# Kernel optimization log

Hardware: AMD Instinct MI355X
Metric: run time of the kernel (lower is better)

Reference implementation:

```python
import jax, jax.numpy as jnp
import numpy as np

SHAPES = [(4, 48, 48), (2, 24, 24), (1, 12, 12), (1, 6, 6)]  # (D,H,W) per level
B, E, NH, NL, NP, DF, NLAYERS = 2, 256, 8, 4, 4, 1024, 6
HD = E // NH
LEVEL_SIZES = [d * h * w for d, h, w in SHAPES]
LEVEL_START = [0] + [int(s) for s in np.cumsum(LEVEL_SIZES)[:-1]]
S = int(sum(LEVEL_SIZES))
PARAM_KEYS = ['W_off', 'b_off', 'W_attn', 'b_attn', 'W_val', 'b_val', 'W_out', 'b_out',
              'ln1_g', 'ln1_b', 'W_ff1', 'b_ff1', 'W_ff2', 'b_ff2', 'ln2_g', 'ln2_b']


def setup_inputs() -> dict:
    key = jax.random.key(0)
    ks = jax.random.split(key, 32)
    inp = {}
    for i, (d, h, w) in enumerate(SHAPES):
        inp[f'feat{i}'] = jax.random.normal(ks[i], (B, E, d, h, w), jnp.float32)
        inp[f'pos{i}'] = jax.random.normal(ks[4 + i], (B, E, d, h, w), jnp.float32)
    inp['level_embed'] = jax.random.normal(ks[8], (NL, E), jnp.float32)
    nrm = lambda k, shape, s: jax.random.normal(k, shape, jnp.float32) * s
    inp['W_off'] = nrm(ks[9], (NLAYERS, E, NH * NL * NP * 3), 0.01)
    inp['b_off'] = nrm(ks[10], (NLAYERS, NH * NL * NP * 3), 1.0)
    inp['W_attn'] = nrm(ks[11], (NLAYERS, E, NH * NL * NP), 0.02)
    inp['b_attn'] = jnp.zeros((NLAYERS, NH * NL * NP), jnp.float32)
    inp['W_val'] = nrm(ks[12], (NLAYERS, E, E), E ** -0.5)
    inp['b_val'] = jnp.zeros((NLAYERS, E), jnp.float32)
    inp['W_out'] = nrm(ks[13], (NLAYERS, E, E), E ** -0.5)
    inp['b_out'] = jnp.zeros((NLAYERS, E), jnp.float32)
    inp['ln1_g'] = jnp.ones((NLAYERS, E), jnp.float32)
    inp['ln1_b'] = jnp.zeros((NLAYERS, E), jnp.float32)
    inp['W_ff1'] = nrm(ks[14], (NLAYERS, E, DF), E ** -0.5)
    inp['b_ff1'] = jnp.zeros((NLAYERS, DF), jnp.float32)
    inp['W_ff2'] = nrm(ks[15], (NLAYERS, DF, E), DF ** -0.5)
    inp['b_ff2'] = jnp.zeros((NLAYERS, E), jnp.float32)
    inp['ln2_g'] = jnp.ones((NLAYERS, E), jnp.float32)
    inp['ln2_b'] = jnp.zeros((NLAYERS, E), jnp.float32)
    return inp


def _layer_norm(x, g, b):
    m = jnp.mean(x, -1, keepdims=True)
    v = jnp.mean((x - m) ** 2, -1, keepdims=True)
    return (x - m) * jax.lax.rsqrt(v + 1e-5) * g + b


def _ref_points():
    # all-zero padding masks -> valid_ratios == 1, so reference points are the
    # normalized voxel centers, identical across levels. Returns (S, 3) in (x, y, z).
    refs = []
    for (D, H, W) in SHAPES:
        z = (jnp.arange(D, dtype=jnp.float32) + 0.5) / D
        y = (jnp.arange(H, dtype=jnp.float32) + 0.5) / H
        x = (jnp.arange(W, dtype=jnp.float32) + 0.5) / W
        zz, yy, xx = jnp.meshgrid(z, y, x, indexing='ij')
        refs.append(jnp.stack([xx.ravel(), yy.ravel(), zz.ravel()], -1))
    return jnp.concatenate(refs, 0)


def _sample_level(v, coords, w, D, H, W):
    # v: (B, NH, N_lvl, HD) flattened level values
    # coords: (B, NH, S, NP, 3) pixel-space coords (x, y, z), align_corners=False convention
    # w: (B, NH, S, NP) attention weights (folded into trilinear corner weights)
    cx, cy, cz = coords[..., 0], coords[..., 1], coords[..., 2]
    x0, y0, z0 = jnp.floor(cx), jnp.floor(cy), jnp.floor(cz)
    fx, fy, fz = cx - x0, cy - y0, cz - z0
    Bq, Hq, Sq, Pq = w.shape
    acc = jnp.zeros((Bq, Hq, Sq, HD), v.dtype)
    for dz in (0, 1):
        wz = fz if dz else 1.0 - fz
        iz = z0 + dz
        for dy in (0, 1):
            wy = fy if dy else 1.0 - fy
            iy = y0 + dy
            for dx in (0, 1):
                wx = fx if dx else 1.0 - fx
                ix = x0 + dx
                valid = (ix >= 0) & (ix < W) & (iy >= 0) & (iy < H) & (iz >= 0) & (iz < D)
                wgt = w * wx * wy * wz * valid  # zero-padding outside the volume
                idx = ((jnp.clip(iz, 0, D - 1) * H + jnp.clip(iy, 0, H - 1)) * W
                       + jnp.clip(ix, 0, W - 1)).astype(jnp.int32)
                g = jnp.take_along_axis(v, idx.reshape(Bq, Hq, Sq * Pq)[..., None], axis=2)
                g = g.reshape(Bq, Hq, Sq, Pq, HD)
                acc = acc + jnp.einsum('bhsp,bhspd->bhsd', wgt, g)
    return acc


def _deform_attn(x, pos, ref, normalizer, p, sample_fn):
    B_, S_, _ = x.shape
    q = x + pos
    value = (x @ p['W_val'] + p['b_val']).reshape(B_, S_, NH, HD).transpose(0, 2, 1, 3)
    off = (q @ p['W_off'] + p['b_off']).reshape(B_, S_, NH, NL, NP, 3)
    attn = jax.nn.softmax((q @ p['W_attn'] + p['b_attn']).reshape(B_, S_, NH, NL * NP), -1)
    attn = attn.reshape(B_, S_, NH, NL, NP)
    # normalized sampling locations in [0,1]^3 (x, y, z)
    loc = ref[None, :, None, None, None, :] + off / normalizer[None, None, None, :, None, :]
    out = jnp.zeros((B_, NH, S_, HD), x.dtype)
    for lvl, (D, H, W) in enumerate(SHAPES):
        s0, n = LEVEL_START[lvl], LEVEL_SIZES[lvl]
        v = value[:, :, s0:s0 + n]
        size = jnp.array([W, H, D], x.dtype)
        coords = (loc[:, :, :, lvl] * size - 0.5).transpose(0, 2, 1, 3, 4)  # (B,NH,S,NP,3)
        w = attn[:, :, :, lvl].transpose(0, 2, 1, 3)  # (B,NH,S,NP)
        out = out + sample_fn(v, coords, w, D, H, W)
    out = out.transpose(0, 2, 1, 3).reshape(B_, S_, E)
    return out @ p['W_out'] + p['b_out']


def _encoder_layer(x, pos, ref, normalizer, p, sample_fn):
    x = _layer_norm(x + _deform_attn(x, pos, ref, normalizer, p, sample_fn),
                    p['ln1_g'], p['ln1_b'])
    h = jax.nn.relu(x @ p['W_ff1'] + p['b_ff1']) @ p['W_ff2'] + p['b_ff2']
    return _layer_norm(x + h, p['ln2_g'], p['ln2_b'])


def _forward(feats, poss, level_embed, params, sample_fn):
    x = jnp.concatenate([f.reshape(f.shape[0], E, -1).transpose(0, 2, 1) for f in feats], axis=1)
    pos = jnp.concatenate(
        [poss[l].reshape(poss[l].shape[0], E, -1).transpose(0, 2, 1) + level_embed[l]
         for l in range(NL)], axis=1)
    ref = _ref_points()
    normalizer = jnp.array([[w, h, d] for d, h, w in SHAPES], jnp.float32)  # (NL,3) (x,y,z)
    for l in range(NLAYERS):
        p = {k: params[k][l] for k in PARAM_KEYS}
        x = _encoder_layer(x, pos, ref, normalizer, p, sample_fn)
    return x


def reference(feat0, feat1, feat2, feat3, pos0, pos1, pos2, pos3, level_embed,
              W_off, b_off, W_attn, b_attn, W_val, b_val, W_out, b_out,
              ln1_g, ln1_b, W_ff1, b_ff1, W_ff2, b_ff2, ln2_g, ln2_b):
    params = dict(W_off=W_off, b_off=b_off, W_attn=W_attn, b_attn=b_attn,
                  W_val=W_val, b_val=b_val, W_out=W_out, b_out=b_out,
                  ln1_g=ln1_g, ln1_b=ln1_b, W_ff1=W_ff1, b_ff1=b_ff1,
                  W_ff2=W_ff2, b_ff2=b_ff2, ln2_g=ln2_g, ln2_b=ln2_b)
    return _forward([feat0, feat1, feat2, feat3], [pos0, pos1, pos2, pos3],
                    level_embed, params, _sample_level)
```

## Files before the change

kernel.cpp:

```cpp
#include <hip/hip_runtime.h>

#define S_TOT   10548
#define M_ROWS  21096
#define M_PAD   21120
#define E_DIM   256
#define NH_DIM  8
#define HD_DIM  32
#define DF_DIM  1024
#define NLAYERS 6

typedef unsigned short ushort_t;
typedef __attribute__((ext_vector_type(8))) short bf16x8;
typedef __attribute__((ext_vector_type(4))) float f32x4;

__device__ inline ushort_t f2bf(float f) {
    unsigned u = __float_as_uint(f);
    u += 0x7FFF + ((u >> 16) & 1);
    return (ushort_t)(u >> 16);
}
__device__ inline float bf2f(ushort_t h) {
    return __uint_as_float(((unsigned)h) << 16);
}
__device__ inline f32x4 up2(unsigned a, unsigned b) {
    f32x4 v;
    v.x = __uint_as_float(a << 16);
    v.y = __uint_as_float(a & 0xffff0000u);
    v.z = __uint_as_float(b << 16);
    v.w = __uint_as_float(b & 0xffff0000u);
    return v;
}
__device__ inline void gload16(const ushort_t* g, ushort_t* l) {
    __builtin_amdgcn_global_load_lds(
        (const __attribute__((address_space(1))) void*)g,
        (__attribute__((address_space(3))) void*)l, 16, 0, 0);
}

__global__ __launch_bounds__(256)
void assemble_kernel(const float* __restrict__ f0, const float* __restrict__ p0,
                     const float* __restrict__ f1, const float* __restrict__ p1,
                     const float* __restrict__ f2, const float* __restrict__ p2,
                     const float* __restrict__ f3, const float* __restrict__ p3,
                     const float* __restrict__ lemb,
                     float* __restrict__ x, ushort_t* __restrict__ posb,
                     ushort_t* __restrict__ xb, ushort_t* __restrict__ qb)
{
    int idx = blockIdx.x * 256 + threadIdx.x;
    int e = idx & (E_DIM - 1);
    int r = idx >> 8;
    int b = (r >= S_TOT) ? 1 : 0;
    int s = r - b * S_TOT;
    const float* f; const float* p; int lvl, j, n;
    if (s < 9216)       { lvl = 0; j = s;         n = 9216; f = f0; p = p0; }
    else if (s < 10368) { lvl = 1; j = s - 9216;  n = 1152; f = f1; p = p1; }
    else if (s < 10512) { lvl = 2; j = s - 10368; n = 144;  f = f2; p = p2; }
    else                { lvl = 3; j = s - 10512; n = 36;   f = f3; p = p3; }
    size_t o = (size_t)(b * E_DIM + e) * n + j;
    float xv = f[o];
    float pv = p[o] + lemb[lvl * E_DIM + e];
    x[idx]    = xv;
    posb[idx] = f2bf(pv);
    xb[idx]   = f2bf(xv);
    qb[idx]   = f2bf(xv + pv);
}

__global__ __launch_bounds__(256)
void transpose_cvt_kernel(const float* __restrict__ src, ushort_t* __restrict__ dst,
                          int K, int N, int dstLayerStride, int dstRowOff)
{
    __shared__ float tile[32][33];
    int l  = blockIdx.z;
    int n0 = blockIdx.x * 32, k0 = blockIdx.y * 32;
    int tx = threadIdx.x & 31, ty = threadIdx.x >> 5;
    const float* s = src + (size_t)l * K * N;
    ushort_t* d    = dst + (size_t)l * dstLayerStride + (size_t)dstRowOff * K;
    #pragma unroll
    for (int i = 0; i < 32; i += 8)
        tile[ty + i][tx] = s[(size_t)(k0 + ty + i) * N + n0 + tx];
    __syncthreads();
    #pragma unroll
    for (int i = 0; i < 32; i += 8)
        d[(size_t)(n0 + ty + i) * K + k0 + tx] = f2bf(tile[tx][ty + i]);
}

__global__ __launch_bounds__(256, 2)
void gemm_part1(const ushort_t* __restrict__ A0, const ushort_t* __restrict__ A1,
                const ushort_t* __restrict__ BtBase,
                const float* __restrict__ b1, const float* __restrict__ b2,
                const float* __restrict__ b3,
                ushort_t* __restrict__ O1, ushort_t* __restrict__ O2,
                ushort_t* __restrict__ O3, int M)
{
    __shared__ short As[2][64 * 32];
    __shared__ short Bs[2][256 * 32];
    const int K = 256;
    int t    = threadIdx.x;
    int sup  = blockIdx.x;
    int row0 = blockIdx.y * 64;
    int lane = t & 63;
    int w    = t >> 6;
    int wn   = w * 64;
    const int quad = lane >> 4, lrow = lane & 15;

    const ushort_t* A  = (sup != 0) ? A1 : A0;
    const ushort_t* Bt = BtBase + (size_t)sup * 256 * K;

    f32x4 acc[4][4];
    #pragma unroll
    for (int i = 0; i < 4; ++i)
        #pragma unroll
        for (int j = 0; j < 4; ++j)
            acc[i][j] = (f32x4){0.f, 0.f, 0.f, 0.f};

    int srow = lane >> 2;
    const int sw = (((lane & 3) ^ ((lane >> 3) & 3)) * 8);
    const int rs = ((quad ^ ((lrow >> 1) & 3)) * 8);
    const ushort_t* Ag = A + (size_t)(row0 + w * 16 + srow) * K + sw;
    const ushort_t* Bg = Bt + (size_t)(w * 64 + srow) * K + sw;

    gload16(Ag, (ushort_t*)&As[0][(w * 16) * 32]);
    #pragma unroll
    for (int q = 0; q < 4; ++q)
        gload16(Bg + (size_t)(q * 16) * K,
                (ushort_t*)&Bs[0][(w * 64 + q * 16) * 32]);

    #pragma unroll
    for (int k0 = 0; k0 < K; k0 += 32) {
        const int cur = (k0 >> 5) & 1;
        __syncthreads();
        if (k0 + 32 < K) {
            const int nxt = cur ^ 1;
            gload16(Ag + k0 + 32, (ushort_t*)&As[nxt][(w * 16) * 32]);
            #pragma unroll
            for (int q = 0; q < 4; ++q)
                gload16(Bg + (size_t)(q * 16) * K + k0 + 32,
                        (ushort_t*)&Bs[nxt][(w * 64 + q * 16) * 32]);
        }
        bf16x8 af[4], bfr[4];
        #pragma unroll
        for (int i = 0; i < 4; ++i)
            af[i] = *(const bf16x8*)&As[cur][(i * 16 + lrow) * 32 + rs];
        #pragma unroll
        for (int j = 0; j < 4; ++j)
            bfr[j] = *(const bf16x8*)&Bs[cur][(wn + j * 16 + lrow) * 32 + rs];
        #pragma unroll
        for (int i = 0; i < 4; ++i)
            #pragma unroll
            for (int j = 0; j < 4; ++j)
                acc[i][j] = __builtin_amdgcn_mfma_f32_16x16x32_bf16(af[i], bfr[j], acc[i][j], 0, 0, 0);
    }

    #pragma unroll
    for (int j = 0; j < 4; ++j) {
        int col = wn + j * 16 + lrow;
        float bia = (sup == 0) ? b1[col]
                  : (sup == 1) ? b2[col]
                  : (col < 128) ? b2[256 + col] : b3[col - 128];
        #pragma unroll
        for (int i = 0; i < 4; ++i)
            #pragma unroll
            for (int rg = 0; rg < 4; ++rg) {
                int row = row0 + i * 16 + quad * 4 + rg;
                if (row < M) {
                    float v = acc[i][j][rg] + bia;
                    if (sup == 0) {
                        int b = (row >= S_TOT) ? 1 : 0;
                        int s = row - b * S_TOT;
                        O1[(((size_t)(b * NH_DIM + (col >> 5))) * S_TOT + s) * HD_DIM + (col & 31)] = f2bf(v);
                    } else if (sup == 2 && col >= 128) {
                        int acol = col - 128;
                        O3[((size_t)(acol >> 4) * M_ROWS + row) * 16 + (acol & 15)] = f2bf(v);
                    } else {
                        int ocol = (sup == 1) ? col : 256 + col;
                        int hh = (ocol * 1366) >> 16;
                        O2[((size_t)hh * M_ROWS + row) * 48 + (ocol - hh * 48)] = f2bf(v);
                    }
                }
            }
    }
}

__global__ __launch_bounds__(256, 2)
void gemm_ln(const ushort_t* __restrict__ A, const ushort_t* __restrict__ Bt,
             const float* __restrict__ bias,
             float* __restrict__ x, ushort_t* __restrict__ xb,
             const float* __restrict__ lng, const float* __restrict__ lnb,
             int M)
{
    __shared__ short As[2][64 * 32];
    __shared__ short Bs[2][256 * 32];
    __shared__ float red1[64 * 5];
    __shared__ float red2[64 * 5];
    const int K = 256;
    int t    = threadIdx.x;
    int row0 = blockIdx.x * 64;
    int lane = t & 63;
    int w    = t >> 6;
    int wn   = w * 64;
    const int quad = lane >> 4, lrow = lane & 15;

    f32x4 acc[4][4];
    #pragma unroll
    for (int i = 0; i < 4; ++i)
        #pragma unroll
        for (int j = 0; j < 4; ++j)
            acc[i][j] = (f32x4){0.f, 0.f, 0.f, 0.f};

    int srow = lane >> 2;
    const int sw = (((lane & 3) ^ ((lane >> 3) & 3)) * 8);
    const int rs = ((quad ^ ((lrow >> 1) & 3)) * 8);
    const ushort_t* Ag = A + (size_t)(row0 + w * 16 + srow) * K + sw;
    const ushort_t* Bg = Bt + (size_t)(w * 64 + srow) * K + sw;

    gload16(Ag, (ushort_t*)&As[0][(w * 16) * 32]);
    #pragma unroll
    for (int q = 0; q < 4; ++q)
        gload16(Bg + (size_t)(q * 16) * K,
                (ushort_t*)&Bs[0][(w * 64 + q * 16) * 32]);

    #pragma unroll
    for (int k0 = 0; k0 < K; k0 += 32) {
        const int cur = (k0 >> 5) & 1;
        __syncthreads();
        if (k0 + 32 < K) {
            const int nxt = cur ^ 1;
            gload16(Ag + k0 + 32, (ushort_t*)&As[nxt][(w * 16) * 32]);
            #pragma unroll
            for (int q = 0; q < 4; ++q)
                gload16(Bg + (size_t)(q * 16) * K + k0 + 32,
                        (ushort_t*)&Bs[nxt][(w * 64 + q * 16) * 32]);
        }
        bf16x8 af[4], bfr[4];
        #pragma unroll
        for (int i = 0; i < 4; ++i)
            af[i] = *(const bf16x8*)&As[cur][(i * 16 + lrow) * 32 + rs];
        #pragma unroll
        for (int j = 0; j < 4; ++j)
            bfr[j] = *(const bf16x8*)&Bs[cur][(wn + j * 16 + lrow) * 32 + rs];
        #pragma unroll
        for (int i = 0; i < 4; ++i)
            #pragma unroll
            for (int j = 0; j < 4; ++j)
                acc[i][j] = __builtin_amdgcn_mfma_f32_16x16x32_bf16(af[i], bfr[j], acc[i][j], 0, 0, 0);
    }

    float gj[4], bj[4], bi[4];
    #pragma unroll
    for (int j = 0; j < 4; ++j) {
        int col = wn + j * 16 + lrow;
        gj[j] = lng[col];
        bj[j] = lnb[col];
        bi[j] = bias[col];
    }

    #pragma unroll
    for (int i = 0; i < 4; ++i)
        #pragma unroll
        for (int rg = 0; rg < 4; ++rg) {
            int row = row0 + i * 16 + quad * 4 + rg;
            #pragma unroll
            for (int j = 0; j < 4; ++j) {
                int col = wn + j * 16 + lrow;
                float xres = (row < M) ? x[(size_t)row * 256 + col] : 0.f;
                acc[i][j][rg] += bi[j] + xres;
            }
            float p1 = acc[i][0][rg] + acc[i][1][rg] + acc[i][2][rg] + acc[i][3][rg];
            float p2 = acc[i][0][rg] * acc[i][0][rg] + acc[i][1][rg] * acc[i][1][rg]
                     + acc[i][2][rg] * acc[i][2][rg] + acc[i][3][rg] * acc[i][3][rg];
            p1 += __shfl_xor(p1, 1); p2 += __shfl_xor(p2, 1);
            p1 += __shfl_xor(p1, 2); p2 += __shfl_xor(p2, 2);
            p1 += __shfl_xor(p1, 4); p2 += __shfl_xor(p2, 4);
            p1 += __shfl_xor(p1, 8); p2 += __shfl_xor(p2, 8);
            if (lrow == 0) {
                int rl = i * 16 + quad * 4 + rg;
                red1[rl * 5 + w] = p1;
                red2[rl * 5 + w] = p2;
            }
        }
    __syncthreads();

    #pragma unroll
    for (int i = 0; i < 4; ++i)
        #pragma unroll
        for (int rg = 0; rg < 4; ++rg) {
            int rl = i * 16 + quad * 4 + rg;
            float S1 = red1[rl * 5 + 0] + red1[rl * 5 + 1] + red1[rl * 5 + 2] + red1[rl * 5 + 3];
            float S2 = red2[rl * 5 + 0] + red2[rl * 5 + 1] + red2[rl * 5 + 2] + red2[rl * 5 + 3];
            float mean = S1 * (1.f / 256);
            float rstd = rsqrtf(S2 * (1.f / 256) - mean * mean + 1e-5f);
            int row = row0 + rl;
            if (row < M) {
                #pragma unroll
                for (int j = 0; j < 4; ++j) {
                    int col = wn + j * 16 + lrow;
                    float out = (acc[i][j][rg] - mean) * rstd * gj[j] + bj[j];
                    size_t o = (size_t)row * 256 + col;
                    x[o]  = out;
                    xb[o] = f2bf(out);
                }
            }
        }
}

__global__ __launch_bounds__(256, 2)
void ffn_kernel(const ushort_t* __restrict__ Axb, const ushort_t* __restrict__ W1t,
                const ushort_t* __restrict__ W2t,
                const float* __restrict__ bias1, const float* __restrict__ bias2,
                float* __restrict__ x, ushort_t* __restrict__ xb,
                ushort_t* __restrict__ qb, const ushort_t* __restrict__ posb,
                const float* __restrict__ lng, const float* __restrict__ lnb,
                int M)
{
    __shared__ short As[2][64 * 32];
    __shared__ short Bs[2][256 * 32];
    __shared__ short Hs[64 * 264];
    __shared__ float red1[64 * 5];
    __shared__ float red2[64 * 5];
    const int K = 256;
    int t    = threadIdx.x;
    int row0 = blockIdx.x * 64;
    int lane = t & 63;
    int w    = t >> 6;
    int wn   = w * 64;
    const int quad = lane >> 4, lrow = lane & 15;
    int srow = lane >> 2;
    const int sw = (((lane & 3) ^ ((lane >> 3) & 3)) * 8);
    const int rs = ((quad ^ ((lrow >> 1) & 3)) * 8);

    f32x4 acc[4][4];
    #pragma unroll
    for (int i = 0; i < 4; ++i)
        #pragma unroll
        for (int j = 0; j < 4; ++j)
            acc[i][j] = (f32x4){0.f, 0.f, 0.f, 0.f};

    const ushort_t* Ag = Axb + (size_t)(row0 + w * 16 + srow) * K + sw;

    for (int c = 0; c < 4; ++c) {
        f32x4 hh[4][4];
        #pragma unroll
        for (int i = 0; i < 4; ++i)
            #pragma unroll
            for (int j = 0; j < 4; ++j)
                hh[i][j] = (f32x4){0.f, 0.f, 0.f, 0.f};

        const ushort_t* B1g = W1t + (size_t)(c * 256 + w * 64 + srow) * K + sw;

        __syncthreads();
        gload16(Ag, (ushort_t*)&As[0][(w * 16) * 32]);
        #pragma unroll
        for (int q = 0; q < 4; ++q)
            gload16(B1g + (size_t)(q * 16) * K,
                    (ushort_t*)&Bs[0][(w * 64 + q * 16) * 32]);

        #pragma unroll
        for (int k0 = 0; k0 < K; k0 += 32) {
            const int cur = (k0 >> 5) & 1;
            __syncthreads();
            if (k0 + 32 < K) {
                const int nxt = cur ^ 1;
                gload16(Ag + k0 + 32, (ushort_t*)&As[nxt][(w * 16) * 32]);
                #pragma unroll
                for (int q = 0; q < 4; ++q)
                    gload16(B1g + (size_t)(q * 16) * K + k0 + 32,
                            (ushort_t*)&Bs[nxt][(w * 64 + q * 16) * 32]);
            }
            bf16x8 af[4], bfr[4];
            #pragma unroll
            for (int i = 0; i < 4; ++i)
                af[i] = *(const bf16x8*)&As[cur][(i * 16 + lrow) * 32 + rs];
            #pragma unroll
            for (int j = 0; j < 4; ++j)
                bfr[j] = *(const bf16x8*)&Bs[cur][(wn + j * 16 + lrow) * 32 + rs];
            #pragma unroll
            for (int i = 0; i < 4; ++i)
                #pragma unroll
                for (int j = 0; j < 4; ++j)
                    hh[i][j] = __builtin_amdgcn_mfma_f32_16x16x32_bf16(af[i], bfr[j], hh[i][j], 0, 0, 0);
        }

        #pragma unroll
        for (int j = 0; j < 4; ++j) {
            int col = wn + j * 16 + lrow;
            float b1v = bias1[c * 256 + col];
            #pragma unroll
            for (int i = 0; i < 4; ++i)
                #pragma unroll
                for (int rg = 0; rg < 4; ++rg) {
                    int rl = i * 16 + quad * 4 + rg;
                    Hs[rl * 264 + col] = f2bf(fmaxf(hh[i][j][rg] + b1v, 0.f));
                }
        }
        __syncthreads();

        const ushort_t* B2g = W2t + (size_t)(w * 64 + srow) * 1024 + c * 256 + sw;
        #pragma unroll
        for (int q = 0; q < 4; ++q)
            gload16(B2g + (size_t)(q * 16) * 1024,
                    (ushort_t*)&Bs[0][(w * 64 + q * 16) * 32]);

        #pragma unroll
        for (int k0 = 0; k0 < 256; k0 += 32) {
            const int cur = (k0 >> 5) & 1;
            __syncthreads();
            if (k0 + 32 < 256) {
                const int nxt = cur ^ 1;
                #pragma unroll
                for (int q = 0; q < 4; ++q)
                    gload16(B2g + (size_t)(q * 16) * 1024 + k0 + 32,
                            (ushort_t*)&Bs[nxt][(w * 64 + q * 16) * 32]);
            }
            bf16x8 af[4], bfr[4];
            #pragma unroll
            for (int i = 0; i < 4; ++i)
                af[i] = *(const bf16x8*)&Hs[(i * 16 + lrow) * 264 + k0 + quad * 8];
            #pragma unroll
            for (int j = 0; j < 4; ++j)
                bfr[j] = *(const bf16x8*)&Bs[cur][(wn + j * 16 + lrow) * 32 + rs];
            #pragma unroll
            for (int i = 0; i < 4; ++i)
                #pragma unroll
                for (int j = 0; j < 4; ++j)
                    acc[i][j] = __builtin_amdgcn_mfma_f32_16x16x32_bf16(af[i], bfr[j], acc[i][j], 0, 0, 0);
        }
    }

    float gj[4], bj[4], bi[4];
    #pragma unroll
    for (int j = 0; j < 4; ++j) {
        int col = wn + j * 16 + lrow;
        gj[j] = lng[col];
        bj[j] = lnb[col];
        bi[j] = bias2[col];
    }

    #pragma unroll
    for (int i = 0; i < 4; ++i)
        #pragma unroll
        for (int rg = 0; rg < 4; ++rg) {
            int row = row0 + i * 16 + quad * 4 + rg;
            #pragma unroll
            for (int j = 0; j < 4; ++j) {
                int col = wn + j * 16 + lrow;
                float xres = (row < M) ? x[(size_t)row * 256 + col] : 0.f;
                acc[i][j][rg] += bi[j] + xres;
            }
            float p1 = acc[i][0][rg] + acc[i][1][rg] + acc[i][2][rg] + acc[i][3][rg];
            float p2 = acc[i][0][rg] * acc[i][0][rg] + acc[i][1][rg] * acc[i][1][rg]
                     + acc[i][2][rg] * acc[i][2][rg] + acc[i][3][rg] * acc[i][3][rg];
            p1 += __shfl_xor(p1, 1); p2 += __shfl_xor(p2, 1);
            p1 += __shfl_xor(p1, 2); p2 += __shfl_xor(p2, 2);
            p1 += __shfl_xor(p1, 4); p2 += __shfl_xor(p2, 4);
            p1 += __shfl_xor(p1, 8); p2 += __shfl_xor(p2, 8);
            if (lrow == 0) {
                int rl = i * 16 + quad * 4 + rg;
                red1[rl * 5 + w] = p1;
                red2[rl * 5 + w] = p2;
            }
        }
    __syncthreads();

    #pragma unroll
    for (int i = 0; i < 4; ++i)
        #pragma unroll
        for (int rg = 0; rg < 4; ++rg) {
            int rl = i * 16 + quad * 4 + rg;
            float S1 = red1[rl * 5 + 0] + red1[rl * 5 + 1] + red1[rl * 5 + 2] + red1[rl * 5 + 3];
            float S2 = red2[rl * 5 + 0] + red2[rl * 5 + 1] + red2[rl * 5 + 2] + red2[rl * 5 + 3];
            float mean = S1 * (1.f / 256);
            float rstd = rsqrtf(S2 * (1.f / 256) - mean * mean + 1e-5f);
            int row = row0 + rl;
            if (row < M) {
                #pragma unroll
                for (int j = 0; j < 4; ++j) {
                    int col = wn + j * 16 + lrow;
                    float out = (acc[i][j][rg] - mean) * rstd * gj[j] + bj[j];
                    size_t o = (size_t)row * 256 + col;
                    x[o]  = out;
                    xb[o] = f2bf(out);
                    qb[o] = f2bf(out + bf2f(posb[o]));
                }
            }
        }
}

__global__ __launch_bounds__(256, 4)
void sample_kernel(const ushort_t* __restrict__ valueb,
                   const ushort_t* __restrict__ offh,
                   const ushort_t* __restrict__ attnh,
                   ushort_t* __restrict__ sampb)
{
    __shared__ float wrec[16 * 168];
    __shared__ int   idxA[16 * 40];

    const int LD_[4]  = {4, 2, 1, 1};
    const int LH_[4]  = {48, 24, 12, 6};
    const int LW_[4]  = {48, 24, 12, 6};
    const int LS0_[4] = {0, 9216, 10368, 10512};

    int t   = threadIdx.x;
    int gl  = t >> 4;
    int sub = t & 15;
    int h   = blockIdx.x;
    int r   = blockIdx.y * 16 + gl;
    bool valid = (r < M_ROWS);
    if (!valid) r = M_ROWS - 1;
    int b   = (r >= S_TOT) ? 1 : 0;
    int s   = r - b * S_TOT;

    float rx, ry, rz;
    {
        int j;
        if (s < 9216)       { j = s;         int qx = j % 48; int q2 = j / 48; int qy = q2 % 48; int qz = q2 / 48;
                              rx = (qx + 0.5f) * (1.f/48); ry = (qy + 0.5f) * (1.f/48); rz = (qz + 0.5f) * (1.f/4); }
        else if (s < 10368) { j = s - 9216;  int qx = j % 24; int q2 = j / 24; int qy = q2 % 24; int qz = q2 / 24;
                              rx = (qx + 0.5f) * (1.f/24); ry = (qy + 0.5f) * (1.f/24); rz = (qz + 0.5f) * (1.f/2); }
        else if (s < 10512) { j = s - 10368; int qx = j % 12; int qy = j / 12;
                              rx = (qx + 0.5f) * (1.f/12); ry = (qy + 0.5f) * (1.f/12); rz = 0.5f; }
        else                { j = s - 10512; int qx = j % 6;  int qy = j / 6;
                              rx = (qx + 0.5f) * (1.f/6);  ry = (qy + 0.5f) * (1.f/6);  rz = 0.5f; }
    }

    {
        int p = sub;
        float lg = bf2f(attnh[((size_t)h * M_ROWS + r) * 16 + p]);
        float mx = lg;
        mx = fmaxf(mx, __shfl_xor(mx, 1));
        mx = fmaxf(mx, __shfl_xor(mx, 2));
        mx = fmaxf(mx, __shfl_xor(mx, 4));
        mx = fmaxf(mx, __shfl_xor(mx, 8));
        float e = __expf(lg - mx);
        float sm = e;
        sm += __shfl_xor(sm, 1);
        sm += __shfl_xor(sm, 2);
        sm += __shfl_xor(sm, 4);
        sm += __shfl_xor(sm, 8);
        float aw = e / sm;

        int lvl = p >> 2;
        const int Dl = LD_[lvl], Hl = LH_[lvl], Wl = LW_[lvl];
        size_t base3 = ((size_t)h * M_ROWS + r) * 48 + p * 3;
        float cx = rx * Wl + bf2f(offh[base3 + 0]) - 0.5f;
        float cy = ry * Hl + bf2f(offh[base3 + 1]) - 0.5f;
        float cz = rz * Dl + bf2f(offh[base3 + 2]) - 0.5f;
        float xf = floorf(cx), yf = floorf(cy), zf = floorf(cz);
        float fx = cx - xf, fy = cy - yf, fz = cz - zf;
        int x0 = (int)xf, y0 = (int)yf, z0 = (int)zf;
        float wx0 = ((unsigned)x0       < (unsigned)Wl) ? 1.f - fx : 0.f;
        float wx1 = ((unsigned)(x0 + 1) < (unsigned)Wl) ? fx       : 0.f;
        float wy0 = ((unsigned)y0       < (unsigned)Hl) ? 1.f - fy : 0.f;
        float wy1 = ((unsigned)(y0 + 1) < (unsigned)Hl) ? fy       : 0.f;
        float wz0 = ((unsigned)z0       < (unsigned)Dl) ? (1.f - fz) * aw : 0.f;
        float wz1 = ((unsigned)(z0 + 1) < (unsigned)Dl) ? fz * aw       : 0.f;
        int xc = min(max(x0, -1), Wl - 1);
        int yc = min(max(y0, -1), Hl - 1);
        int zc = min(max(z0, -1), Dl - 1);
        int idx = LS0_[lvl] + (zc * Hl + yc) * Wl + xc;

        float* wp = &wrec[gl * 168 + p * 8];
        *(f32x4*)wp       = (f32x4){wz0 * wy0 * wx0, wz0 * wy0 * wx1,
                                    wz0 * wy1 * wx0, wz0 * wy1 * wx1};
        *(f32x4*)(wp + 4) = (f32x4){wz1 * wy0 * wx0, wz1 * wy0 * wx1,
                                    wz1 * wy1 * wx0, wz1 * wy1 * wx1};
        idxA[gl * 40 + p] = idx;
    }
    __syncthreads();

    int q  = sub & 3;
    int cr = sub >> 2;
    int dy = cr >> 1, dx = cr & 1;
    const ushort_t* vb = valueb + ((size_t)(b * NH_DIM + h) * S_TOT) * HD_DIM + q * 8;
    f32x4 accA = (f32x4){0.f, 0.f, 0.f, 0.f};
    f32x4 accB = (f32x4){0.f, 0.f, 0.f, 0.f};

    #pragma unroll
    for (int p = 0; p < 16; ++p) {
        const int lvl = p >> 2;
        const int Wl = LW_[lvl];
        const int HW = LH_[lvl] * LW_[lvl];
        float w0 = wrec[gl * 168 + p * 8 + cr];
        float w1 = wrec[gl * 168 + p * 8 + 4 + cr];
        int idx = idxA[gl * 40 + p] + dy * Wl + dx;
        const ushort_t* cb = vb + (long long)idx * HD_DIM;
        uint4 u0 = *(const uint4*)cb;
        uint4 u1 = *(const uint4*)(cb + HW * HD_DIM);
        accA += w0 * up2(u0.x, u0.y);
        accB += w0 * up2(u0.z, u0.w);
        accA += w1 * up2(u1.x, u1.y);
        accB += w1 * up2(u1.z, u1.w);
    }

    accA.x += __shfl_xor(accA.x, 4); accA.y += __shfl_xor(accA.y, 4);
    accA.z += __shfl_xor(accA.z, 4); accA.w += __shfl_xor(accA.w, 4);
    accB.x += __shfl_xor(accB.x, 4); accB.y += __shfl_xor(accB.y, 4);
    accB.z += __shfl_xor(accB.z, 4); accB.w += __shfl_xor(accB.w, 4);
    accA.x += __shfl_xor(accA.x, 8); accA.y += __shfl_xor(accA.y, 8);
    accA.z += __shfl_xor(accA.z, 8); accA.w += __shfl_xor(accA.w, 8);
    accB.x += __shfl_xor(accB.x, 8); accB.y += __shfl_xor(accB.y, 8);
    accB.z += __shfl_xor(accB.z, 8); accB.w += __shfl_xor(accB.w, 8);

    if (cr == 0 && valid) {
        ushort4 o1, o2;
        o1.x = f2bf(accA.x); o1.y = f2bf(accA.y); o1.z = f2bf(accA.z); o1.w = f2bf(accA.w);
        o2.x = f2bf(accB.x); o2.y = f2bf(accB.y); o2.z = f2bf(accB.z); o2.w = f2bf(accB.w);
        ushort_t* op = sampb + (size_t)r * E_DIM + h * HD_DIM + q * 8;
        *(ushort4*)op       = o1;
        *(ushort4*)(op + 4) = o2;
    }
}

extern "C" void kernel_launch(void* const* d_in, const int* in_sizes, int n_in,
                              void* d_out, int out_size, void* d_ws, size_t ws_size,
                              hipStream_t stream)
{
    const float* f0     = (const float*)d_in[0];
    const float* p0     = (const float*)d_in[1];
    const float* f1     = (const float*)d_in[2];
    const float* p1     = (const float*)d_in[3];
    const float* f2     = (const float*)d_in[4];
    const float* p2     = (const float*)d_in[5];
    const float* f3     = (const float*)d_in[6];
    const float* p3     = (const float*)d_in[7];
    const float* lemb   = (const float*)d_in[8];
    const float* W_off  = (const float*)d_in[9];
    const float* b_off  = (const float*)d_in[10];
    const float* W_attn = (const float*)d_in[11];
    const float* b_attn = (const float*)d_in[12];
    const float* W_val  = (const float*)d_in[13];
    const float* b_val  = (const float*)d_in[14];
    const float* W_out  = (const float*)d_in[15];
    const float* b_out  = (const float*)d_in[16];
    const float* ln1_g  = (const float*)d_in[17];
    const float* ln1_b  = (const float*)d_in[18];
    const float* W_ff1  = (const float*)d_in[19];
    const float* b_ff1  = (const float*)d_in[20];
    const float* W_ff2  = (const float*)d_in[21];
    const float* b_ff2  = (const float*)d_in[22];
    const float* ln2_g  = (const float*)d_in[23];
    const float* ln2_b  = (const float*)d_in[24];

    float* x = (float*)d_out;
    char*  w = (char*)d_ws;

    ushort_t* posb   = (ushort_t*)(w + 0);
    ushort_t* valueb = (ushort_t*)(w + 21626880 + 262144);
    char*     region =            (w + 34525184);
    ushort_t* offh   = (ushort_t*)(region);
    ushort_t* attnh  = (ushort_t*)(region + 16220160);
    ushort_t* sampb  = (ushort_t*)(region + 21626880);
    ushort_t* xb     = (ushort_t*)(w + 77778944);
    ushort_t* qb     = (ushort_t*)(w + 88592384);
    ushort_t* wb     = (ushort_t*)(w + 99405824);

    ushort_t* Wc_t = wb;
    ushort_t* Wp_t = wb + 1179648;
    ushort_t* W1_t = wb + 1572864;
    ushort_t* W2_t = wb + 3145728;

    dim3 blk(256);

    transpose_cvt_kernel<<<dim3(8, 8, 6),  blk, 0, stream>>>(W_val,  Wc_t, 256, 256,  196608, 0);
    transpose_cvt_kernel<<<dim3(12, 8, 6), blk, 0, stream>>>(W_off,  Wc_t, 256, 384,  196608, 256);
    transpose_cvt_kernel<<<dim3(4, 8, 6),  blk, 0, stream>>>(W_attn, Wc_t, 256, 128,  196608, 640);
    transpose_cvt_kernel<<<dim3(8, 8, 6),  blk, 0, stream>>>(W_out,  Wp_t, 256, 256,   65536, 0);
    transpose_cvt_kernel<<<dim3(32, 8, 6), blk, 0, stream>>>(W_ff1,  W1_t, 256, 1024, 262144, 0);
    transpose_cvt_kernel<<<dim3(8, 32, 6), blk, 0, stream>>>(W_ff2,  W2_t, 1024, 256, 262144, 0);

    assemble_kernel<<<(M_ROWS * E_DIM) / 256, blk, 0, stream>>>(
        f0, p0, f1, p1, f2, p2, f3, p3, lemb, x, posb, xb, qb);

    const int MT = M_PAD / 64;
    const int SB = (M_ROWS + 15) / 16;
    for (int l = 0; l < NLAYERS; ++l) {
        gemm_part1<<<dim3(3, MT), blk, 0, stream>>>(
            xb, qb, Wc_t + l * 196608,
            b_val + l * 256, b_off + l * 384, b_attn + l * 128,
            valueb, offh, attnh, M_ROWS);
        sample_kernel<<<dim3(NH_DIM, SB), blk, 0, stream>>>(valueb, offh, attnh, sampb);
        gemm_ln<<<MT, blk, 0, stream>>>(
            sampb, Wp_t + l * 65536, b_out + l * 256,
            x, xb, ln1_g + l * 256, ln1_b + l * 256, M_ROWS);
        ffn_kernel<<<MT, blk, 0, stream>>>(
            xb, W1_t + l * 262144, W2_t + l * 262144,
            b_ff1 + l * 1024, b_ff2 + l * 256,
            x, xb, qb, posb,
            ln2_g + l * 256, ln2_b + l * 256, M_ROWS);
    }
}
```

Measured before the change: 1.168 ms.

## Halve row tile in LN GEMM and FFN kernels, tile-transpose input assembly

The row tile of gemm_ln and ffn_kernel drops from 64 to 32 rows. This halves accumulators and LDS use, reuses the A buffer for the reduction scratch, raises the occupancy hint to 4 blocks, and doubles the grid so more blocks cover the CUs. The assemble kernel now does an LDS-tiled transpose, so reads from the channel-major feature and pos tensors are coalesced. The price is that each weight tile is reused across fewer rows, so weight traffic from L2 grows.

```diff
diff --git a/kernel.cpp b/kernel.cpp
--- a/kernel.cpp
+++ b/kernel.cpp
@@ -44,23 +44,49 @@
                      float* __restrict__ x, ushort_t* __restrict__ posb,
                      ushort_t* __restrict__ xb, ushort_t* __restrict__ qb)
 {
-    int idx = blockIdx.x * 256 + threadIdx.x;
-    int e = idx & (E_DIM - 1);
-    int r = idx >> 8;
-    int b = (r >= S_TOT) ? 1 : 0;
-    int s = r - b * S_TOT;
-    const float* f; const float* p; int lvl, j, n;
-    if (s < 9216)       { lvl = 0; j = s;         n = 9216; f = f0; p = p0; }
-    else if (s < 10368) { lvl = 1; j = s - 9216;  n = 1152; f = f1; p = p1; }
-    else if (s < 10512) { lvl = 2; j = s - 10368; n = 144;  f = f2; p = p2; }
-    else                { lvl = 3; j = s - 10512; n = 36;   f = f3; p = p3; }
-    size_t o = (size_t)(b * E_DIM + e) * n + j;
-    float xv = f[o];
-    float pv = p[o] + lemb[lvl * E_DIM + e];
-    x[idx]    = xv;
-    posb[idx] = f2bf(pv);
-    xb[idx]   = f2bf(xv);
-    qb[idx]   = f2bf(xv + pv);
+    __shared__ float tf[32][33];
+    __shared__ float tp[32][33];
+
+    int tb = blockIdx.x;
+    int e0 = blockIdx.y * 32;
+    int b  = blockIdx.z;
+    int lvl, j0, n, s0; const float* f; const float* p;
+    if (tb < 288)      { lvl = 0; j0 = tb * 32;         n = 9216; s0 = 0;     f = f0; p = p0; }
+    else if (tb < 324) { lvl = 1; j0 = (tb - 288) * 32; n = 1152; s0 = 9216;  f = f1; p = p1; }
+    else if (tb < 329) { lvl = 2; j0 = (tb - 324) * 32; n = 144;  s0 = 10368; f = f2; p = p2; }
+    else               { lvl = 3; j0 = (tb - 329) * 32; n = 36;   s0 = 10512; f = f3; p = p3; }
+
+    int tx = threadIdx.x & 31, ty = threadIdx.x >> 5;
+    bool jv = (j0 + tx) < n;
+    size_t base = (size_t)(b * E_DIM + e0) * n + j0 + tx;
+    #pragma unroll
+    for (int i = 0; i < 4; ++i) {
+        int e = ty + i * 8;
+        float fv = 0.f, pv = 0.f;
+        if (jv) {
+            fv = f[base + (size_t)e * n];
+            pv = p[base + (size_t)e * n];
+        }
+        tf[e][tx] = fv;
+        tp[e][tx] = pv;
+    }
+    __syncthreads();
+
+    float lv = lemb[lvl * E_DIM + e0 + tx];
+    #pragma unroll
+    for (int i = 0; i < 4; ++i) {
+        int jl = ty + i * 8;
+        if (j0 + jl < n) {
+            int r = b * S_TOT + s0 + j0 + jl;
+            float xv = tf[tx][jl];
+            float pv = tp[tx][jl] + lv;
+            size_t o = (size_t)r * E_DIM + e0 + tx;
+            x[o]    = xv;
+            posb[o] = f2bf(pv);
+            xb[o]   = f2bf(xv);
+            qb[o]   = f2bf(xv + pv);
+        }
+    }
 }
 
 __global__ __launch_bounds__(256)
@@ -179,28 +205,28 @@
     }
 }
 
-__global__ __launch_bounds__(256, 2)
+__global__ __launch_bounds__(256, 4)
 void gemm_ln(const ushort_t* __restrict__ A, const ushort_t* __restrict__ Bt,
              const float* __restrict__ bias,
              float* __restrict__ x, ushort_t* __restrict__ xb,
              const float* __restrict__ lng, const float* __restrict__ lnb,
              int M)
 {
-    __shared__ short As[2][64 * 32];
+    __shared__ short As[2][32 * 32];
     __shared__ short Bs[2][256 * 32];
-    __shared__ float red1[64 * 5];
-    __shared__ float red2[64 * 5];
+    float* red1 = (float*)&As[0][0];
+    float* red2 = red1 + 32 * 5;
     const int K = 256;
     int t    = threadIdx.x;
-    int row0 = blockIdx.x * 64;
+    int row0 = blockIdx.x * 32;
     int lane = t & 63;
     int w    = t >> 6;
     int wn   = w * 64;
     const int quad = lane >> 4, lrow = lane & 15;
 
-    f32x4 acc[4][4];
-    #pragma unroll
-    for (int i = 0; i < 4; ++i)
+    f32x4 acc[2][4];
+    #pragma unroll
+    for (int i = 0; i < 2; ++i)
         #pragma unroll
         for (int j = 0; j < 4; ++j)
             acc[i][j] = (f32x4){0.f, 0.f, 0.f, 0.f};
@@ -211,7 +237,7 @@
     const ushort_t* Ag = A + (size_t)(row0 + w * 16 + srow) * K + sw;
     const ushort_t* Bg = Bt + (size_t)(w * 64 + srow) * K + sw;
 
-    gload16(Ag, (ushort_t*)&As[0][(w * 16) * 32]);
+    if (w < 2) gload16(Ag, (ushort_t*)&As[0][(w * 16) * 32]);
     #pragma unroll
     for (int q = 0; q < 4; ++q)
         gload16(Bg + (size_t)(q * 16) * K,
@@ -223,21 +249,21 @@
         __syncthreads();
         if (k0 + 32 < K) {
             const int nxt = cur ^ 1;
-            gload16(Ag + k0 + 32, (ushort_t*)&As[nxt][(w * 16) * 32]);
+            if (w < 2) gload16(Ag + k0 + 32, (ushort_t*)&As[nxt][(w * 16) * 32]);
             #pragma unroll
             for (int q = 0; q < 4; ++q)
                 gload16(Bg + (size_t)(q * 16) * K + k0 + 32,
                         (ushort_t*)&Bs[nxt][(w * 64 + q * 16) * 32]);
         }
-        bf16x8 af[4], bfr[4];
-        #pragma unroll
-        for (int i = 0; i < 4; ++i)
+        bf16x8 af[2], bfr[4];
+        #pragma unroll
+        for (int i = 0; i < 2; ++i)
             af[i] = *(const bf16x8*)&As[cur][(i * 16 + lrow) * 32 + rs];
         #pragma unroll
         for (int j = 0; j < 4; ++j)
             bfr[j] = *(const bf16x8*)&Bs[cur][(wn + j * 16 + lrow) * 32 + rs];
         #pragma unroll
-        for (int i = 0; i < 4; ++i)
+        for (int i = 0; i < 2; ++i)
             #pragma unroll
             for (int j = 0; j < 4; ++j)
                 acc[i][j] = __builtin_amdgcn_mfma_f32_16x16x32_bf16(af[i], bfr[j], acc[i][j], 0, 0, 0);
@@ -253,7 +279,7 @@
     }
 
     #pragma unroll
-    for (int i = 0; i < 4; ++i)
+    for (int i = 0; i < 2; ++i)
         #pragma unroll
         for (int rg = 0; rg < 4; ++rg) {
             int row = row0 + i * 16 + quad * 4 + rg;
@@ -279,7 +305,7 @@
     __syncthreads();
 
     #pragma unroll
-    for (int i = 0; i < 4; ++i)
+    for (int i = 0; i < 2; ++i)
         #pragma unroll
         for (int rg = 0; rg < 4; ++rg) {
             int rl = i * 16 + quad * 4 + rg;
@@ -310,14 +336,14 @@
                 const float* __restrict__ lng, const float* __restrict__ lnb,
                 int M)
 {
-    __shared__ short As[2][64 * 32];
+    __shared__ short As[2][32 * 32];
     __shared__ short Bs[2][256 * 32];
-    __shared__ short Hs[64 * 264];
-    __shared__ float red1[64 * 5];
-    __shared__ float red2[64 * 5];
+    __shared__ short Hs[32 * 264];
+    float* red1 = (float*)&As[0][0];
+    float* red2 = red1 + 32 * 5;
     const int K = 256;
     int t    = threadIdx.x;
-    int row0 = blockIdx.x * 64;
+    int row0 = blockIdx.x * 32;
     int lane = t & 63;
     int w    = t >> 6;
     int wn   = w * 64;
@@ -326,9 +352,9 @@
     const int sw = (((lane & 3) ^ ((lane >> 3) & 3)) * 8);
     const int rs = ((quad ^ ((lrow >> 1) & 3)) * 8);
 
-    f32x4 acc[4][4];
-    #pragma unroll
-    for (int i = 0; i < 4; ++i)
+    f32x4 acc[2][4];
+    #pragma unroll
+    for (int i = 0; i < 2; ++i)
         #pragma unroll
         for (int j = 0; j < 4; ++j)
             acc[i][j] = (f32x4){0.f, 0.f, 0.f, 0.f};
@@ -336,9 +362,9 @@
     const ushort_t* Ag = Axb + (size_t)(row0 + w * 16 + srow) * K + sw;
 
     for (int c = 0; c < 4; ++c) {
-        f32x4 hh[4][4];
-        #pragma unroll
-        for (int i = 0; i < 4; ++i)
+        f32x4 hh[2][4];
+        #pragma unroll
+        for (int i = 0; i < 2; ++i)
             #pragma unroll
             for (int j = 0; j < 4; ++j)
                 hh[i][j] = (f32x4){0.f, 0.f, 0.f, 0.f};
@@ -346,7 +372,7 @@
         const ushort_t* B1g = W1t + (size_t)(c * 256 + w * 64 + srow) * K + sw;
 
         __syncthreads();
-        gload16(Ag, (ushort_t*)&As[0][(w * 16) * 32]);
+        if (w < 2) gload16(Ag, (ushort_t*)&As[0][(w * 16) * 32]);
         #pragma unroll
         for (int q = 0; q < 4; ++q)
             gload16(B1g + (size_t)(q * 16) * K,
@@ -358,21 +384,21 @@
             __syncthreads();
             if (k0 + 32 < K) {
                 const int nxt = cur ^ 1;
-                gload16(Ag + k0 + 32, (ushort_t*)&As[nxt][(w * 16) * 32]);
+                if (w < 2) gload16(Ag + k0 + 32, (ushort_t*)&As[nxt][(w * 16) * 32]);
                 #pragma unroll
                 for (int q = 0; q < 4; ++q)
                     gload16(B1g + (size_t)(q * 16) * K + k0 + 32,
                             (ushort_t*)&Bs[nxt][(w * 64 + q * 16) * 32]);
             }
-            bf16x8 af[4], bfr[4];
-            #pragma unroll
-            for (int i = 0; i < 4; ++i)
+            bf16x8 af[2], bfr[4];
+            #pragma unroll
+            for (int i = 0; i < 2; ++i)
                 af[i] = *(const bf16x8*)&As[cur][(i * 16 + lrow) * 32 + rs];
             #pragma unroll
             for (int j = 0; j < 4; ++j)
                 bfr[j] = *(const bf16x8*)&Bs[cur][(wn + j * 16 + lrow) * 32 + rs];
             #pragma unroll
-            for (int i = 0; i < 4; ++i)
+            for (int i = 0; i < 2; ++i)
                 #pragma unroll
                 for (int j = 0; j < 4; ++j)
                     hh[i][j] = __builtin_amdgcn_mfma_f32_16x16x32_bf16(af[i], bfr[j], hh[i][j], 0, 0, 0);
@@ -383,7 +409,7 @@
             int col = wn + j * 16 + lrow;
             float b1v = bias1[c * 256 + col];
             #pragma unroll
-            for (int i = 0; i < 4; ++i)
+            for (int i = 0; i < 2; ++i)
                 #pragma unroll
                 for (int rg = 0; rg < 4; ++rg) {
                     int rl = i * 16 + quad * 4 + rg;
@@ -409,15 +435,15 @@
                     gload16(B2g + (size_t)(q * 16) * 1024 + k0 + 32,
                             (ushort_t*)&Bs[nxt][(w * 64 + q * 16) * 32]);
             }
-            bf16x8 af[4], bfr[4];
-            #pragma unroll
-            for (int i = 0; i < 4; ++i)
+            bf16x8 af[2], bfr[4];
+            #pragma unroll
+            for (int i = 0; i < 2; ++i)
                 af[i] = *(const bf16x8*)&Hs[(i * 16 + lrow) * 264 + k0 + quad * 8];
             #pragma unroll
             for (int j = 0; j < 4; ++j)
                 bfr[j] = *(const bf16x8*)&Bs[cur][(wn + j * 16 + lrow) * 32 + rs];
             #pragma unroll
-            for (int i = 0; i < 4; ++i)
+            for (int i = 0; i < 2; ++i)
                 #pragma unroll
                 for (int j = 0; j < 4; ++j)
                     acc[i][j] = __builtin_amdgcn_mfma_f32_16x16x32_bf16(af[i], bfr[j], acc[i][j], 0, 0, 0);
@@ -434,7 +460,7 @@
     }
 
     #pragma unroll
-    for (int i = 0; i < 4; ++i)
+    for (int i = 0; i < 2; ++i)
         #pragma unroll
         for (int rg = 0; rg < 4; ++rg) {
             int row = row0 + i * 16 + quad * 4 + rg;
@@ -460,7 +486,7 @@
     __syncthreads();
 
     #pragma unroll
-    for (int i = 0; i < 4; ++i)
+    for (int i = 0; i < 2; ++i)
         #pragma unroll
         for (int rg = 0; rg < 4; ++rg) {
             int rl = i * 16 + quad * 4 + rg;
@@ -665,10 +691,11 @@
     transpose_cvt_kernel<<<dim3(32, 8, 6), blk, 0, stream>>>(W_ff1,  W1_t, 256, 1024, 262144, 0);
     transpose_cvt_kernel<<<dim3(8, 32, 6), blk, 0, stream>>>(W_ff2,  W2_t, 1024, 256, 262144, 0);
 
-    assemble_kernel<<<(M_ROWS * E_DIM) / 256, blk, 0, stream>>>(
+    assemble_kernel<<<dim3(331, 8, 2), blk, 0, stream>>>(
         f0, p0, f1, p1, f2, p2, f3, p3, lemb, x, posb, xb, qb);
 
     const int MT = M_PAD / 64;
+    const int LT = M_PAD / 32;
     const int SB = (M_ROWS + 15) / 16;
     for (int l = 0; l < NLAYERS; ++l) {
         gemm_part1<<<dim3(3, MT), blk, 0, stream>>>(
@@ -676,10 +703,10 @@
             b_val + l * 256, b_off + l * 384, b_attn + l * 128,
             valueb, offh, attnh, M_ROWS);
         sample_kernel<<<dim3(NH_DIM, SB), blk, 0, stream>>>(valueb, offh, attnh, sampb);
-        gemm_ln<<<MT, blk, 0, stream>>>(
+        gemm_ln<<<LT, blk, 0, stream>>>(
             sampb, Wp_t + l * 65536, b_out + l * 256,
             x, xb, ln1_g + l * 256, ln1_b + l * 256, M_ROWS);
-        ffn_kernel<<<MT, blk, 0, stream>>>(
+        ffn_kernel<<<LT, blk, 0, stream>>>(
             xb, W1_t + l * 262144, W2_t + l * 262144,
             b_ff1 + l * 1024, b_ff2 + l * 256,
             x, xb, qb, posb,
```

Measured after the change: 1.116 ms. -4.5%, faster.
